# Performance work log

Measured on AMD Instinct MI355X. Metric: run time of the kernel, lower is better.

## Reference

```python
import jax, jax.numpy as jnp
import numpy as np

EPS = 1e-06


def _cross(a, b):
    return a[..., 0] * b[..., 1] - a[..., 1] * b[..., 0]


def box2corners(box):
    # box: (N,5) = x, y, w, h, alpha -> corners (N,4,2), CCW order
    x, y, w, h, a = (box[:, i] for i in range(5))
    x4 = jnp.array([0.5, -0.5, -0.5, 0.5], box.dtype) * w[:, None]
    y4 = jnp.array([0.5, 0.5, -0.5, -0.5], box.dtype) * h[:, None]
    c, s = jnp.cos(a)[:, None], jnp.sin(a)[:, None]
    return jnp.stack([x4 * c - y4 * s + x[:, None],
                      x4 * s + y4 * c + y[:, None]], axis=-1)


def box_intersection(c1, c2):
    # all 4x4 edge-pair segment intersections; returns (N,16,2) points, (N,16) valid mask
    p1 = c1[:, :, None, :]
    d1 = (jnp.roll(c1, -1, axis=1) - c1)[:, :, None, :]
    p2 = c2[:, None, :, :]
    d2 = (jnp.roll(c2, -1, axis=1) - c2)[:, None, :, :]
    den = _cross(d1, d2)                       # (N,4,4)
    safe = jnp.abs(den) > 1e-12
    den_s = jnp.where(safe, den, 1.0)
    dp = p2 - p1
    t = _cross(dp, d2) / den_s
    u = _cross(dp, d1) / den_s
    mask = safe & (t > 0) & (t < 1) & (u > 0) & (u < 1)
    pts = jnp.where(mask[..., None], p1 + t[..., None] * d1, 0.0)
    n = c1.shape[0]
    return pts.reshape(n, 16, 2), mask.reshape(n, 16)


def box_in_box(c1, c2):
    # which corners of box1 lie inside rectangle box2 (projection test)
    a = c2[:, 0:1]
    ab = c2[:, 1:2] - a
    ad = c2[:, 3:4] - a
    am = c1 - a
    pab = jnp.sum(am * ab, -1) / jnp.maximum(jnp.sum(ab * ab, -1), EPS)
    pad = jnp.sum(am * ad, -1) / jnp.maximum(jnp.sum(ad * ad, -1), EPS)
    tol = 1e-6
    return (pab > -tol) & (pab < 1 + tol) & (pad > -tol) & (pad < 1 + tol)


def intersection_area(c1, c2):
    # candidate vertices: corners of each box inside the other + edge intersections
    ipts, imask = box_intersection(c1, c2)
    v = jnp.concatenate([c1, c2, ipts], axis=1)                      # (N,24,2)
    m = jnp.concatenate([box_in_box(c1, c2), box_in_box(c2, c1), imask], axis=1)
    nv = jnp.sum(m, axis=-1)                                         # num valid
    mf = m.astype(v.dtype)[..., None]
    mean = jnp.sum(v * mf, axis=1) / jnp.maximum(nv, 1)[:, None]
    r = (v - mean[:, None]) * mf                                     # invalid -> 0
    # sort valid vertices CCW by angle around centroid (invalid pushed to end)
    ang = jnp.where(m, jnp.arctan2(r[..., 1], r[..., 0]), 1e6)
    order = jnp.argsort(ang, axis=-1)
    rs = jnp.take_along_axis(r, order[..., None], axis=1)            # (N,24,2)
    # shoelace over consecutive pairs; invalid entries are zero so contribute 0
    area2 = jnp.sum(_cross(rs[:, :-1], rs[:, 1:]), axis=1)
    # closure term: last valid vertex -> first vertex
    idx = jnp.broadcast_to(jnp.maximum(nv - 1, 0)[:, None, None], (v.shape[0], 1, 2))
    r_last = jnp.take_along_axis(rs, idx, axis=1)[:, 0]
    area2 = area2 + _cross(r_last, rs[:, 0])
    return 0.5 * jnp.abs(area2)


def setup_inputs() -> dict:
    key = jax.random.key(0)
    k1, k2, k3, k4, k5 = jax.random.split(key, 5)
    N = 1_000_000
    cxy = jax.random.uniform(k1, (N, 2), jnp.float32) * 1024.0
    wh = jax.random.uniform(k2, (N, 2), jnp.float32) * 60.0 + 4.0
    ang = jax.random.uniform(k3, (N, 1), jnp.float32) * jnp.pi
    pred = jnp.concatenate([cxy, wh, ang], axis=1)
    noise = jax.random.normal(k4, (N, 5), jnp.float32) * jnp.array([3.0, 3.0, 2.0, 2.0, 0.1], jnp.float32)
    target = pred + noise
    target = target.at[:, 2:4].set(jnp.clip(target[:, 2:4], 1.0))
    weight = jax.random.uniform(k5, (N,), jnp.float32)
    return {"pred": pred, "target": target, "weight": weight}


def reference(pred, target, weight):
    loss_weight = 1.0
    c1 = box2corners(pred)
    c2 = box2corners(target)
    inter = intersection_area(c1, c2)
    a1 = pred[:, 2] * pred[:, 3]
    a2 = target[:, 2] * target[:, 3]
    ious = jnp.clip(inter / (a1 + a2 - inter), EPS)
    center_distance = (pred[:, 0] - target[:, 0]) ** 2 + (pred[:, 1] - target[:, 1]) ** 2
    aspect = (4.0 / jnp.pi ** 2) * (jnp.arctan(target[:, 2] / (target[:, 3] + EPS))
                                    - jnp.arctan(pred[:, 2] / (pred[:, 3] + EPS))) ** 2
    v = aspect / (1.0 - ious + aspect)
    alpha = v / (1.0 - ious + v)
    loss = 1.0 - ious + center_distance / (pred[:, 2] ** 2 + pred[:, 3] ** 2 + EPS) + alpha * v
    # weighted_loss with weight, reduction='mean', avg_factor=None
    return loss_weight * jnp.mean(loss * weight)
```

## Files before the change

kernel.cpp:

```cpp
#include <hip/hip_runtime.h>
#include <math.h>

#define EPSF 1e-6f

__device__ __forceinline__ float block_reduce_sum(float v) {
    #pragma unroll
    for (int off = 32; off > 0; off >>= 1)
        v += __shfl_down(v, off, 64);
    __shared__ float smem[4];
    int lane = threadIdx.x & 63;
    int wid  = threadIdx.x >> 6;
    if (lane == 0) smem[wid] = v;
    __syncthreads();
    float s = 0.0f;
    if (threadIdx.x == 0) {
        #pragma unroll
        for (int w = 0; w < 4; w++) s += smem[w];
    }
    return s;
}

__global__ void __launch_bounds__(256)
ciou_loss_kernel(const float* __restrict__ pred,
                 const float* __restrict__ target,
                 const float* __restrict__ weight,
                 float* __restrict__ partial,
                 int N)
{
    int tid = threadIdx.x;
    int idx = blockIdx.x * 256 + tid;
    float contrib = 0.0f;
    if (idx < N) {
        const float* p = pred   + (size_t)idx * 5;
        const float* t = target + (size_t)idx * 5;
        float px = p[0], py = p[1], pw = p[2], ph = p[3], pa = p[4];
        float tx = t[0], ty = t[1], tw = t[2], th = t[3], ta = t[4];

        float cx0 = 0.5f * (px + tx), cy0 = 0.5f * (py + ty);

        const float sgx[4] = { 0.5f, -0.5f, -0.5f,  0.5f };
        const float sgy[4] = { 0.5f,  0.5f, -0.5f, -0.5f };
        float Pxv[4], Pyv[4], Qxv[4], Qyv[4];
        float ca, sa, cb, sb;
        __sincosf(pa, &sa, &ca);
        __sincosf(ta, &sb, &cb);
        #pragma unroll
        for (int i = 0; i < 4; i++) {
            float x4 = sgx[i] * pw, y4 = sgy[i] * ph;
            Pxv[i] = x4 * ca - y4 * sa + (px - cx0);
            Pyv[i] = x4 * sa + y4 * ca + (py - cy0);
            float u4 = sgx[i] * tw, v4 = sgy[i] * th;
            Qxv[i] = u4 * cb - v4 * sb + (tx - cx0);
            Qyv[i] = u4 * sb + v4 * cb + (ty - cy0);
        }

        float Pex[4], Pey[4], Qex[4], Qey[4];
        #pragma unroll
        for (int i = 0; i < 4; i++) {
            Pex[i] = Pxv[(i + 1) & 3] - Pxv[i];
            Pey[i] = Pyv[(i + 1) & 3] - Pyv[i];
            Qex[i] = Qxv[(i + 1) & 3] - Qxv[i];
            Qey[i] = Qyv[(i + 1) & 3] - Qyv[i];
        }

        float dPQ[4][4], dQP[4][4];
        #pragma unroll
        for (int i = 0; i < 4; i++) {
            #pragma unroll
            for (int j = 0; j < 4; j++) {
                dPQ[i][j] = Qex[j] * (Pyv[i] - Qyv[j]) - Qey[j] * (Pxv[i] - Qxv[j]);
                dQP[i][j] = Pex[j] * (Qyv[i] - Pyv[j]) - Pey[j] * (Qxv[i] - Pxv[j]);
            }
        }

        float area2 = 0.0f;

        #pragma unroll
        for (int i = 0; i < 4; i++) {
            int ip = (i + 1) & 3;
            float Cx = Pxv[i], Cy = Pyv[i];
            float ex = Pex[i], ey = Pey[i];
            float t0 = 0.0f, t1 = 1.0f;
            #pragma unroll
            for (int j = 0; j < 4; j++) {
                float dc = dPQ[i][j], dd = dPQ[ip][j];
                float denom = dc - dd;
                bool  par   = fabsf(denom) < 1e-12f;
                float ds    = par ? 1.0f : denom;
                float tt    = dc * __builtin_amdgcn_rcpf(ds);
                bool  enter = denom < 0.0f;
                t0 = (!par &&  enter) ? fmaxf(t0, tt) : t0;
                t1 = (!par && !enter) ? fminf(t1, tt) : t1;
                t1 = (par && dc < 0.0f) ? -1.0f : t1;
            }
            float t1c = fmaxf(t1, t0);
            float Ax = Cx + t0  * ex, Ay = Cy + t0  * ey;
            float Bx = Cx + t1c * ex, By = Cy + t1c * ey;
            area2 += Ax * By - Ay * Bx;
        }

        #pragma unroll
        for (int i = 0; i < 4; i++) {
            int ip = (i + 1) & 3;
            float Cx = Qxv[i], Cy = Qyv[i];
            float ex = Qex[i], ey = Qey[i];
            float t0 = 0.0f, t1 = 1.0f;
            #pragma unroll
            for (int j = 0; j < 4; j++) {
                float dc = dQP[i][j], dd = dQP[ip][j];
                float denom = dc - dd;
                bool  par   = fabsf(denom) < 1e-12f;
                float ds    = par ? 1.0f : denom;
                float tt    = dc * __builtin_amdgcn_rcpf(ds);
                bool  enter = denom < 0.0f;
                t0 = (!par &&  enter) ? fmaxf(t0, tt) : t0;
                t1 = (!par && !enter) ? fminf(t1, tt) : t1;
                t1 = (par && dc < 0.0f) ? -1.0f : t1;
            }
            float t1c = fmaxf(t1, t0);
            float Ax = Cx + t0  * ex, Ay = Cy + t0  * ey;
            float Bx = Cx + t1c * ex, By = Cy + t1c * ey;
            area2 += Ax * By - Ay * Bx;
        }

        float inter = 0.5f * fabsf(area2);

        float a1 = pw * ph, a2 = tw * th;
        float iou = inter / (a1 + a2 - inter);
        iou = fmaxf(iou, EPSF);
        float dx0 = px - tx, dy0 = py - ty;
        float cd = dx0 * dx0 + dy0 * dy0;
        float da = atanf(tw / (th + EPSF)) - atanf(pw / (ph + EPSF));
        const float c4pi2 = 4.0f / (3.14159265358979323846f * 3.14159265358979323846f);
        float aspect = c4pi2 * da * da;
        float vterm = aspect / (1.0f - iou + aspect);
        float alpha = vterm / (1.0f - iou + vterm);
        float loss = 1.0f - iou + cd / (pw * pw + ph * ph + EPSF) + alpha * vterm;
        contrib = loss * weight[idx];
    }

    float s = block_reduce_sum(contrib);
    if (threadIdx.x == 0) partial[blockIdx.x] = s;
}

__global__ void __launch_bounds__(256)
reduce_final_kernel(const float* __restrict__ partial, int nparts, float invN,
                    float* __restrict__ out)
{
    float s = 0.0f;
    for (int i = threadIdx.x; i < nparts; i += 256) s += partial[i];
    s = block_reduce_sum(s);
    if (threadIdx.x == 0) out[0] = s * invN;
}

extern "C" void kernel_launch(void* const* d_in, const int* in_sizes, int n_in,
                              void* d_out, int out_size, void* d_ws, size_t ws_size,
                              hipStream_t stream) {
    const float* pred   = (const float*)d_in[0];
    const float* target = (const float*)d_in[1];
    const float* weight = (const float*)d_in[2];
    int N = in_sizes[2];
    float* partial = (float*)d_ws;

    int blocks = (N + 255) / 256;
    ciou_loss_kernel<<<blocks, 256, 0, stream>>>(pred, target, weight, partial, N);
    reduce_final_kernel<<<1, 256, 0, stream>>>(partial, blocks, 1.0f / (float)N,
                                               (float*)d_out);
}
```

Measured before the change: 102.8 us.

## Simplify clip-area math, use fast atan difference, widen final reduction

Clip-segment area accumulation now uses the precomputed edge cross products (t1-t0)*cross(Ci,Ci+1) instead of explicit endpoints. Half-plane distances come from fma with per-edge constants, and the parallel-edge special case is replaced by a clamped denominator. The two atanf calls become one polynomial atan of (u-v)/(1+uv). The final reduction kernel uses 1024 threads. These cut ALU work, but the polynomial atan and the dropped parallel-edge handling can shift results slightly.

```diff
diff --git a/kernel.cpp b/kernel.cpp
--- a/kernel.cpp
+++ b/kernel.cpp
@@ -3,11 +3,12 @@
 
 #define EPSF 1e-6f
 
+template <int NWAVES>
 __device__ __forceinline__ float block_reduce_sum(float v) {
     #pragma unroll
     for (int off = 32; off > 0; off >>= 1)
         v += __shfl_down(v, off, 64);
-    __shared__ float smem[4];
+    __shared__ float smem[NWAVES];
     int lane = threadIdx.x & 63;
     int wid  = threadIdx.x >> 6;
     if (lane == 0) smem[wid] = v;
@@ -15,9 +16,26 @@
     float s = 0.0f;
     if (threadIdx.x == 0) {
         #pragma unroll
-        for (int w = 0; w < 4; w++) s += smem[w];
+        for (int w = 0; w < NWAVES; w++) s += smem[w];
     }
     return s;
+}
+
+__device__ __forceinline__ float fast_atan(float x) {
+    const float a1  =  0.99997726f, a3 = -0.33262347f, a5  =  0.19354346f,
+                a7  = -0.11643287f, a9 =  0.05265332f, a11 = -0.01172120f;
+    float ax  = fabsf(x);
+    bool  big = ax > 1.0f;
+    float z   = big ? __builtin_amdgcn_rcpf(ax) : ax;
+    float z2  = z * z;
+    float p   = fmaf(z2, a11, a9);
+    p = fmaf(z2, p, a7);
+    p = fmaf(z2, p, a5);
+    p = fmaf(z2, p, a3);
+    p = fmaf(z2, p, a1);
+    float r = z * p;
+    r = big ? (1.57079632679f - r) : r;
+    return copysignf(r, x);
 }
 
 __global__ void __launch_bounds__(256)
@@ -35,6 +53,7 @@
         const float* t = target + (size_t)idx * 5;
         float px = p[0], py = p[1], pw = p[2], ph = p[3], pa = p[4];
         float tx = t[0], ty = t[1], tw = t[2], th = t[3], ta = t[4];
+        float wgt = weight[idx];
 
         float cx0 = 0.5f * (px + tx), cy0 = 0.5f * (py + ty);
 
@@ -54,73 +73,70 @@
             Qyv[i] = u4 * sb + v4 * cb + (ty - cy0);
         }
 
-        float Pex[4], Pey[4], Qex[4], Qey[4];
+        float Pex[4], Pey[4], Qex[4], Qey[4], cP[4], cQ[4];
         #pragma unroll
         for (int i = 0; i < 4; i++) {
-            Pex[i] = Pxv[(i + 1) & 3] - Pxv[i];
-            Pey[i] = Pyv[(i + 1) & 3] - Pyv[i];
-            Qex[i] = Qxv[(i + 1) & 3] - Qxv[i];
-            Qey[i] = Qyv[(i + 1) & 3] - Qyv[i];
-        }
-
-        float dPQ[4][4], dQP[4][4];
-        #pragma unroll
-        for (int i = 0; i < 4; i++) {
-            #pragma unroll
-            for (int j = 0; j < 4; j++) {
-                dPQ[i][j] = Qex[j] * (Pyv[i] - Qyv[j]) - Qey[j] * (Pxv[i] - Qxv[j]);
-                dQP[i][j] = Pex[j] * (Qyv[i] - Pyv[j]) - Pey[j] * (Qxv[i] - Pxv[j]);
-            }
+            int ip = (i + 1) & 3;
+            Pex[i] = Pxv[ip] - Pxv[i];
+            Pey[i] = Pyv[ip] - Pyv[i];
+            Qex[i] = Qxv[ip] - Qxv[i];
+            Qey[i] = Qyv[ip] - Qyv[i];
+            cP[i]  = Pxv[i] * Pyv[ip] - Pyv[i] * Pxv[ip];
+            cQ[i]  = Qxv[i] * Qyv[ip] - Qyv[i] * Qxv[ip];
         }
 
         float area2 = 0.0f;
 
-        #pragma unroll
-        for (int i = 0; i < 4; i++) {
-            int ip = (i + 1) & 3;
-            float Cx = Pxv[i], Cy = Pyv[i];
-            float ex = Pex[i], ey = Pey[i];
-            float t0 = 0.0f, t1 = 1.0f;
+        {
+            float d[4][4];
             #pragma unroll
-            for (int j = 0; j < 4; j++) {
-                float dc = dPQ[i][j], dd = dPQ[ip][j];
-                float denom = dc - dd;
-                bool  par   = fabsf(denom) < 1e-12f;
-                float ds    = par ? 1.0f : denom;
-                float tt    = dc * __builtin_amdgcn_rcpf(ds);
-                bool  enter = denom < 0.0f;
-                t0 = (!par &&  enter) ? fmaxf(t0, tt) : t0;
-                t1 = (!par && !enter) ? fminf(t1, tt) : t1;
-                t1 = (par && dc < 0.0f) ? -1.0f : t1;
+            for (int i = 0; i < 4; i++)
+                #pragma unroll
+                for (int j = 0; j < 4; j++)
+                    d[i][j] = fmaf(Qex[j], Pyv[i], fmaf(-Qey[j], Pxv[i], cQ[j]));
+
+            #pragma unroll
+            for (int i = 0; i < 4; i++) {
+                int ip = (i + 1) & 3;
+                float t0 = 0.0f, t1 = 1.0f;
+                #pragma unroll
+                for (int j = 0; j < 4; j++) {
+                    float dc = d[i][j], dd = d[ip][j];
+                    float denom = dc - dd;
+                    float ds = copysignf(fmaxf(fabsf(denom), 1e-12f), denom);
+                    float tt = dc * __builtin_amdgcn_rcpf(ds);
+                    bool  enter = denom < 0.0f;
+                    t0 = fmaxf(t0, enter ? tt : 0.0f);
+                    t1 = fminf(t1, enter ? 1.0f : tt);
+                }
+                area2 = fmaf(fmaxf(t1, t0) - t0, cP[i], area2);
             }
-            float t1c = fmaxf(t1, t0);
-            float Ax = Cx + t0  * ex, Ay = Cy + t0  * ey;
-            float Bx = Cx + t1c * ex, By = Cy + t1c * ey;
-            area2 += Ax * By - Ay * Bx;
         }
 
-        #pragma unroll
-        for (int i = 0; i < 4; i++) {
-            int ip = (i + 1) & 3;
-            float Cx = Qxv[i], Cy = Qyv[i];
-            float ex = Qex[i], ey = Qey[i];
-            float t0 = 0.0f, t1 = 1.0f;
+        {
+            float d[4][4];
             #pragma unroll
-            for (int j = 0; j < 4; j++) {
-                float dc = dQP[i][j], dd = dQP[ip][j];
-                float denom = dc - dd;
-                bool  par   = fabsf(denom) < 1e-12f;
-                float ds    = par ? 1.0f : denom;
-                float tt    = dc * __builtin_amdgcn_rcpf(ds);
-                bool  enter = denom < 0.0f;
-                t0 = (!par &&  enter) ? fmaxf(t0, tt) : t0;
-                t1 = (!par && !enter) ? fminf(t1, tt) : t1;
-                t1 = (par && dc < 0.0f) ? -1.0f : t1;
+            for (int i = 0; i < 4; i++)
+                #pragma unroll
+                for (int j = 0; j < 4; j++)
+                    d[i][j] = fmaf(Pex[j], Qyv[i], fmaf(-Pey[j], Qxv[i], cP[j]));
+
+            #pragma unroll
+            for (int i = 0; i < 4; i++) {
+                int ip = (i + 1) & 3;
+                float t0 = 0.0f, t1 = 1.0f;
+                #pragma unroll
+                for (int j = 0; j < 4; j++) {
+                    float dc = d[i][j], dd = d[ip][j];
+                    float denom = dc - dd;
+                    float ds = copysignf(fmaxf(fabsf(denom), 1e-12f), denom);
+                    float tt = dc * __builtin_amdgcn_rcpf(ds);
+                    bool  enter = denom < 0.0f;
+                    t0 = fmaxf(t0, enter ? tt : 0.0f);
+                    t1 = fminf(t1, enter ? 1.0f : tt);
+                }
+                area2 = fmaf(fmaxf(t1, t0) - t0, cQ[i], area2);
             }
-            float t1c = fmaxf(t1, t0);
-            float Ax = Cx + t0  * ex, Ay = Cy + t0  * ey;
-            float Bx = Cx + t1c * ex, By = Cy + t1c * ey;
-            area2 += Ax * By - Ay * Bx;
         }
 
         float inter = 0.5f * fabsf(area2);
@@ -130,26 +146,28 @@
         iou = fmaxf(iou, EPSF);
         float dx0 = px - tx, dy0 = py - ty;
         float cd = dx0 * dx0 + dy0 * dy0;
-        float da = atanf(tw / (th + EPSF)) - atanf(pw / (ph + EPSF));
+        float u  = tw * __builtin_amdgcn_rcpf(th + EPSF);
+        float v  = pw * __builtin_amdgcn_rcpf(ph + EPSF);
+        float da = fast_atan((u - v) * __builtin_amdgcn_rcpf(fmaf(u, v, 1.0f)));
         const float c4pi2 = 4.0f / (3.14159265358979323846f * 3.14159265358979323846f);
         float aspect = c4pi2 * da * da;
         float vterm = aspect / (1.0f - iou + aspect);
         float alpha = vterm / (1.0f - iou + vterm);
         float loss = 1.0f - iou + cd / (pw * pw + ph * ph + EPSF) + alpha * vterm;
-        contrib = loss * weight[idx];
+        contrib = loss * wgt;
     }
 
-    float s = block_reduce_sum(contrib);
+    float s = block_reduce_sum<4>(contrib);
     if (threadIdx.x == 0) partial[blockIdx.x] = s;
 }
 
-__global__ void __launch_bounds__(256)
+__global__ void __launch_bounds__(1024)
 reduce_final_kernel(const float* __restrict__ partial, int nparts, float invN,
                     float* __restrict__ out)
 {
     float s = 0.0f;
-    for (int i = threadIdx.x; i < nparts; i += 256) s += partial[i];
-    s = block_reduce_sum(s);
+    for (int i = threadIdx.x; i < nparts; i += 1024) s += partial[i];
+    s = block_reduce_sum<16>(s);
     if (threadIdx.x == 0) out[0] = s * invN;
 }
 
@@ -164,6 +182,6 @@
 
     int blocks = (N + 255) / 256;
     ciou_loss_kernel<<<blocks, 256, 0, stream>>>(pred, target, weight, partial, N);
-    reduce_final_kernel<<<1, 256, 0, stream>>>(partial, blocks, 1.0f / (float)N,
-                                               (float*)d_out);
+    reduce_final_kernel<<<1, 1024, 0, stream>>>(partial, blocks, 1.0f / (float)N,
+                                                (float*)d_out);
 }
```

Result: faster. 96.28 us (-6.4%).
